# Performance work log

Hardware: AMD Instinct MI355X
Metric: run time of the kernel (lower is better)

Reference implementation:

```python
import jax, jax.numpy as jnp
import numpy as np

_EPS = 1e-5
RC = 5.0   # cutoff radius
L = 20     # number of radial basis functions
N = 10000  # nodes
E = 100000 # edges
F = 128    # in_feats


def _ssp(x):
    # ShiftedSoftplus: softplus(x) - log(2)
    return jax.nn.softplus(x) - jnp.log(2.0)


def _rbf(r):
    # DimeNet radial basis: sqrt(2/rc) * sin(n*pi*r/rc) / r, n = 1..L.  r: [E,1] -> [E,L]
    n = jnp.arange(1, L + 1, dtype=r.dtype)
    return jnp.sqrt(2.0 / RC) * jnp.sin(n * jnp.pi * r / RC) / r


def _fc(u):
    # cosine cutoff applied elementwise: 0.5*(cos(pi*u/rc)+1) for u < rc else 0
    return jnp.where(u < RC, 0.5 * (jnp.cos(jnp.pi * u / RC) + 1.0), 0.0)


def setup_inputs() -> dict:
    key = jax.random.key(0)
    ks = jax.random.split(key, 12)

    def nrm(k, shape, scale=1.0):
        return jax.random.normal(k, shape, dtype=jnp.float32) * scale

    return {
        "x": nrm(ks[0], (N, 3)) * 3.0,           # atomic positions
        "v": nrm(ks[1], (N, F, 3)),               # vector node features
        "s": nrm(ks[2], (N, F)),                  # scalar node features
        "ms1_w": nrm(ks[3], (F, F), F ** -0.5),
        "ms1_b": jnp.zeros((F,), jnp.float32),
        "ms2_w": nrm(ks[4], (3 * F, F), F ** -0.5),
        "ms2_b": jnp.zeros((3 * F,), jnp.float32),
        "mv_w": nrm(ks[5], (3 * F, L), L ** -0.5),
        "mv_b": jnp.zeros((3 * F,), jnp.float32),
        "us1_w": nrm(ks[6], (F, F), F ** -0.5),
        "us1_b": jnp.zeros((F,), jnp.float32),
        "us2_w": nrm(ks[7], (3 * F, F), F ** -0.5),
        "us2_b": jnp.zeros((3 * F,), jnp.float32),
        "src": jax.random.randint(ks[8], (E,), 0, N, dtype=jnp.int32),
        "dst": jax.random.randint(ks[9], (E,), 0, N, dtype=jnp.int32),
    }


def reference(x, v, s, ms1_w, ms1_b, ms2_w, ms2_b, mv_w, mv_b,
              us1_w, us1_b, us2_w, us2_b, src, dst):
    # ---------- pass 1: message1 + reduce1 (sum over incoming edges) ----------
    sj = s[src]                                   # [E,F]   src scalar features
    vj = v[src]                                   # [E,F,3] src vector features
    vec = x[src] - x[dst]                         # [E,3]   x_i - x_j (molecule branch)
    r = jnp.sqrt(jnp.sum(vec ** 2, axis=-1) + _EPS)[:, None]          # [E,1]
    phi = _ssp(sj @ ms1_w.T + ms1_b) @ ms2_w.T + ms2_b                 # [E,3F]
    w = _fc(_rbf(r) @ mv_w.T + mv_b)                                    # [E,3F]
    v_, s_, r_ = jnp.split(phi * w, 3, axis=-1)                         # each [E,F]
    dv_e = vj * v_[:, :, None] + r_[:, :, None] * (vec / r)[:, None, :] # [E,F,3]
    dv = jax.ops.segment_sum(dv_e, dst, num_segments=N)                 # [N,F,3]
    ds = jax.ops.segment_sum(s_, dst, num_segments=N)                   # [N,F]
    v_new = v + dv
    s_new = s + ds

    # ---------- pass 2: message2 + reduce2 (mean over incoming edges) ----------
    s2 = _ssp(s_new[src] @ us1_w.T + us1_b) @ us2_w.T + us2_b           # [E,3F]
    deg = jax.ops.segment_sum(jnp.ones((E,), s.dtype), dst, num_segments=N)
    denom = jnp.maximum(deg, 1.0)
    s_mean = jax.ops.segment_sum(s2, dst, num_segments=N) / denom[:, None]        # [N,3F]
    uv = jax.ops.segment_sum(v_new[src], dst, num_segments=N) / denom[:, None, None]  # [N,F,3]
    avv, asv, ass = jnp.split(s_mean, 3, axis=-1)                       # each [N,F]
    norm = jnp.sqrt(jnp.sum(uv ** 2, axis=-1) + _EPS)[..., None]        # [N,F,1]
    dv2 = uv * avv[:, :, None]                                           # [N,F,3]
    ds2 = jnp.sum((uv / norm) ** 2, axis=-1) * asv + ass                 # [N,F]
    return (v_new + dv2, s_new + ds2)
```

## Files before the change

### kernel.cpp

```cpp
#include <hip/hip_runtime.h>
#include <hip/hip_bf16.h>


#define F_DIM   128
#define F3_DIM  384
#define L_DIM   20
#define CAP     64

typedef __attribute__((ext_vector_type(8))) short short8;
typedef __attribute__((ext_vector_type(4))) float f32x4;
typedef __attribute__((ext_vector_type(4))) unsigned short us4;

__device__ __forceinline__ unsigned short f2bf(float f) {
  union { float f; unsigned u; } a; a.f = f;
  unsigned u = a.u;
  u = (u + 0x7FFFu + ((u >> 16) & 1u)) >> 16;
  return (unsigned short)u;
}
__device__ __forceinline__ float bf2f(unsigned short u) {
  union { unsigned u; float f; } a; a.u = ((unsigned)u) << 16;
  return a.f;
}

__global__ __launch_bounds__(256) void cast_kernel(
    const float* __restrict__ ms1_w, unsigned short* __restrict__ w_ms1,
    const float* __restrict__ ms2_w, unsigned short* __restrict__ w_ms2,
    const float* __restrict__ us1_w, unsigned short* __restrict__ w_us1,
    const float* __restrict__ us2_w, unsigned short* __restrict__ w_us2,
    const float* __restrict__ s,     unsigned short* __restrict__ sbf,
    const float* __restrict__ v,     us4* __restrict__ v4,
    const float* __restrict__ mv_w,  unsigned short* __restrict__ mvwB,
    int nF)
{
  int i = blockIdx.x * 256 + threadIdx.x;
  if (i < 16384) w_ms1[i] = f2bf(ms1_w[i]);
  if (i < 49152) w_ms2[i] = f2bf(ms2_w[i]);
  if (i < 16384) w_us1[i] = f2bf(us1_w[i]);
  if (i < 49152) w_us2[i] = f2bf(us2_w[i]);
  if (i < nF)    sbf[i] = f2bf(s[i]);
  if (i < nF) {
    const float* vp = v + (size_t)i * 3;
    us4 o; o.x = f2bf(vp[0]); o.y = f2bf(vp[1]); o.z = f2bf(vp[2]); o.w = 0;
    v4[i] = o;
  }
  if (i < 384 * 32) {
    int o = i >> 5, k = i & 31;
    float val = (k < 20) ? mv_w[o * 20 + k] * 0.6324555320336759f : 0.f;
    mvwB[i] = f2bf(val);
  }
}

__global__ __launch_bounds__(256) void fill_kernel(
    const int* __restrict__ src, const int* __restrict__ dst,
    int* __restrict__ cursor, int* __restrict__ jbuf, int E)
{
  int e = blockIdx.x * 256 + threadIdx.x;
  if (e < E) {
    int d = dst[e];
    int p = atomicAdd(&cursor[d], 1);
    if (p < CAP) jbuf[d * CAP + p] = src[e];
  }
}

__global__ __launch_bounds__(64) void mlp_kernel(
    const unsigned short* __restrict__ X,
    const unsigned short* __restrict__ W1,
    const float* __restrict__ B1,
    const unsigned short* __restrict__ W2,
    const float* __restrict__ B2,
    unsigned short* __restrict__ Yp)
{
  __shared__ float HT[128 * 17];
  const int lane = threadIdx.x;
  const int c    = lane & 15;
  const int quad = lane >> 4;
  const int m0   = blockIdx.x * 16;

  f32x4 acc[8];
#pragma unroll
  for (int t = 0; t < 8; t++) acc[t] = (f32x4){0.f, 0.f, 0.f, 0.f};
#pragma unroll
  for (int kk = 0; kk < 4; kk++) {
    short8 a = *(const short8*)(X + (size_t)(m0 + c) * 128 + kk * 32 + quad * 8);
#pragma unroll
    for (int t = 0; t < 8; t++) {
      short8 b = *(const short8*)(W1 + (size_t)(t * 16 + c) * 128 + kk * 32 + quad * 8);
      acc[t] = __builtin_amdgcn_mfma_f32_16x16x32_bf16(a, b, acc[t], 0, 0, 0);
    }
  }
#pragma unroll
  for (int t = 0; t < 8; t++) {
    float bias = B1[t * 16 + c];
    int k = t * 16 + c;
#pragma unroll
    for (int r = 0; r < 4; r++) {
      float h = acc[t][r] + bias;
      float sp = (h > 15.f) ? h : log1pf(__expf(h));
      sp -= 0.69314718056f;
      HT[k * 17 + quad * 4 + r] = sp;
    }
  }
  __syncthreads();

  for (int g = 0; g < 3; g++) {
    f32x4 acc2[8];
#pragma unroll
    for (int t = 0; t < 8; t++) acc2[t] = (f32x4){0.f, 0.f, 0.f, 0.f};
#pragma unroll
    for (int kk = 0; kk < 4; kk++) {
      short8 afr;
#pragma unroll
      for (int j = 0; j < 8; j++) {
        float hv = HT[(kk * 32 + quad * 8 + j) * 17 + c];
        afr[j] = (short)f2bf(hv);
      }
#pragma unroll
      for (int t = 0; t < 8; t++) {
        short8 b = *(const short8*)(W2 + (size_t)(g * 128 + t * 16 + c) * 128 + kk * 32 + quad * 8);
        acc2[t] = __builtin_amdgcn_mfma_f32_16x16x32_bf16(afr, b, acc2[t], 0, 0, 0);
      }
    }
#pragma unroll
    for (int t = 0; t < 8; t++) {
      int f = t * 16 + c;
      float bias = B2[g * 128 + f];
#pragma unroll
      for (int r = 0; r < 4; r++) {
        int m = quad * 4 + r;
        Yp[(size_t)(m0 + m) * 512 + f * 4 + g] = f2bf(acc2[t][r] + bias);
      }
    }
  }
}

__global__ __launch_bounds__(256, 4) void pass1_kernel(
    const float* __restrict__ x,
    const us4*  __restrict__ phi4,
    const us4*  __restrict__ v4,
    const float* __restrict__ v,
    const float* __restrict__ s,
    const unsigned short* __restrict__ mvwB,
    const float* __restrict__ mv_b,
    const int* __restrict__ jbuf,
    const int* __restrict__ deg,
    float* __restrict__ vnew, us4* __restrict__ vnew4,
    float* __restrict__ snew, unsigned short* __restrict__ snew_bf, int nNodes)
{
  __shared__ unsigned short Asn[32 * 32];
  __shared__ float4 Au[32];
  __shared__ us4 Wl[32 * 128];
  __shared__ float red[512];

  const int tid  = threadIdx.x;
  const int wave = tid >> 6, lane = tid & 63;
  const int half = wave >> 1, split = wave & 1;
  const int i = blockIdx.x;
  const int f = lane + 64 * half;
  const int c = lane & 15, quad = lane >> 4;

  int cnt = deg[i]; if (cnt > CAP) cnt = CAP;
  const int base = i * CAP;

  short8 bfr[6]; float bias[6];
#pragma unroll
  for (int p = 0; p < 3; p++)
#pragma unroll
    for (int h = 0; h < 2; h++) {
      int t = 2 * wave + h + 8 * p;
      bfr[p * 2 + h]  = *(const short8*)(mvwB + (size_t)(t * 16 + c) * 32 + quad * 8);
      bias[p * 2 + h] = mv_b[t * 16 + c];
    }

  const float xi0 = x[i * 3], xi1 = x[i * 3 + 1], xi2 = x[i * 3 + 2];
  int jv = (lane < cnt) ? jbuf[base + lane] : 0;

  float accV0 = 0.f, accV1 = 0.f, accV2 = 0.f, accS = 0.f;

  for (int bs = 0; bs < cnt; bs += 32) {
    int bcnt = cnt - bs; if (bcnt > 32) bcnt = 32;
    __syncthreads();

    if (tid < 32) {
      int e = bs + tid;
      if (e < cnt) {
        int j = jbuf[base + e];
        float d0 = x[j * 3]     - xi0;
        float d1 = x[j * 3 + 1] - xi1;
        float d2 = x[j * 3 + 2] - xi2;
        float r = sqrtf(d0 * d0 + d1 * d1 + d2 * d2 + 1e-5f);
        float invr = 1.0f / r;
        Au[tid] = make_float4(d0 * invr, d1 * invr, d2 * invr, invr);
        float theta = r * 0.6283185307179586f;
        float s1, c1;
        __sincosf(theta, &s1, &c1);
        float c2 = 2.f * c1;
        float pm2 = s1, pm1 = c2 * s1;
        Asn[tid * 32 + 0] = f2bf(pm2);
        Asn[tid * 32 + 1] = f2bf(pm1);
#pragma unroll
        for (int l = 2; l < L_DIM; l++) {
          float cur = c2 * pm1 - pm2;
          Asn[tid * 32 + l] = f2bf(cur);
          pm2 = pm1; pm1 = cur;
        }
#pragma unroll
        for (int l = L_DIM; l < 32; l++) Asn[tid * 32 + l] = 0;
      }
    }
    __syncthreads();

    int nrg = (bcnt + 15) >> 4;
    for (int rg = 0; rg < nrg; rg++) {
      short8 a = *(const short8*)&Asn[(rg * 16 + c) * 32 + quad * 8];
      f32x4 acc[6];
#pragma unroll
      for (int q = 0; q < 6; q++)
        acc[q] = __builtin_amdgcn_mfma_f32_16x16x32_bf16(
            a, bfr[q], (f32x4){0.f, 0.f, 0.f, 0.f}, 0, 0, 0);
#pragma unroll
      for (int r = 0; r < 4; r++) {
        int el = rg * 16 + quad * 4 + r;
        if (el < bcnt) {
          float invr = Au[el].w;
#pragma unroll
          for (int h = 0; h < 2; h++) {
            float wp0 = fmaf(acc[h][r],     invr, bias[h]);
            float wp1 = fmaf(acc[2 + h][r], invr, bias[2 + h]);
            float wp2 = fmaf(acc[4 + h][r], invr, bias[4 + h]);
            float w0 = (wp0 < 5.f) ? 0.5f * (__cosf(wp0 * 0.6283185307179586f) + 1.f) : 0.f;
            float w1 = (wp1 < 5.f) ? 0.5f * (__cosf(wp1 * 0.6283185307179586f) + 1.f) : 0.f;
            float w2 = (wp2 < 5.f) ? 0.5f * (__cosf(wp2 * 0.6283185307179586f) + 1.f) : 0.f;
            us4 o; o.x = f2bf(w0); o.y = f2bf(w1); o.z = f2bf(w2); o.w = 0;
            Wl[el * 128 + wave * 32 + h * 16 + c] = o;
          }
        }
      }
    }
    __syncthreads();

    for (int e = split; e < bcnt; e += 2) {
      int j = __shfl(jv, bs + e);
      float4 u = Au[e];
      us4 wv = Wl[e * 128 + f];
      us4 pv = phi4[(size_t)j * 128 + f];
      us4 vv = v4[(size_t)j * 128 + f];
      float m0 = bf2f(pv.x) * bf2f(wv.x);
      float m1 = bf2f(pv.y) * bf2f(wv.y);
      float m2 = bf2f(pv.z) * bf2f(wv.z);
      accV0 = fmaf(bf2f(vv.x), m0, fmaf(m2, u.x, accV0));
      accV1 = fmaf(bf2f(vv.y), m0, fmaf(m2, u.y, accV1));
      accV2 = fmaf(bf2f(vv.z), m0, fmaf(m2, u.z, accV2));
      accS += m1;
    }
  }

  const int idx = half * 64 + lane;
  __syncthreads();
  if (split == 1) {
    red[idx * 4 + 0] = accV0; red[idx * 4 + 1] = accV1;
    red[idx * 4 + 2] = accV2; red[idx * 4 + 3] = accS;
  }
  __syncthreads();
  if (split == 0) {
    accV0 += red[idx * 4 + 0]; accV1 += red[idx * 4 + 1];
    accV2 += red[idx * 4 + 2]; accS  += red[idx * 4 + 3];
    size_t b3 = (size_t)i * 384 + f * 3;
    float n0 = v[b3] + accV0, n1 = v[b3 + 1] + accV1, n2 = v[b3 + 2] + accV2;
    vnew[b3] = n0; vnew[b3 + 1] = n1; vnew[b3 + 2] = n2;
    us4 o; o.x = f2bf(n0); o.y = f2bf(n1); o.z = f2bf(n2); o.w = 0;
    vnew4[(size_t)i * 128 + f] = o;
    size_t b1 = (size_t)i * 128 + f;
    float sv = s[b1] + accS;
    snew[b1] = sv;
    snew_bf[b1] = f2bf(sv);
  }
}

__global__ __launch_bounds__(256, 8) void pass2_kernel(
    const float* __restrict__ vnew,
    const us4*  __restrict__ vnew4,
    const float* __restrict__ snew,
    const us4*  __restrict__ s2p,
    const int* __restrict__ jbuf, const int* __restrict__ deg,
    float* __restrict__ vout, float* __restrict__ sout, int nNodes)
{
  __shared__ float red[1024];
  const int wave = threadIdx.x >> 6, lane = threadIdx.x & 63;
  const int half = wave >> 1, split = wave & 1;
  const int i = blockIdx.x;
  const int f = lane + 64 * half;

  int cnt = deg[i]; if (cnt > CAP) cnt = CAP;
  const int base = i * CAP;
  int jv = (lane < cnt) ? jbuf[base + lane] : 0;

  float accU0 = 0.f, accU1 = 0.f, accU2 = 0.f;
  float accM0 = 0.f, accM1 = 0.f, accM2 = 0.f;

#pragma unroll 2
  for (int e = split; e < cnt; e += 2) {
    int j = __shfl(jv, e);
    us4 sm = s2p[(size_t)j * 128 + f];
    us4 vm = vnew4[(size_t)j * 128 + f];
    accM0 += bf2f(sm.x); accM1 += bf2f(sm.y); accM2 += bf2f(sm.z);
    accU0 += bf2f(vm.x); accU1 += bf2f(vm.y); accU2 += bf2f(vm.z);
  }

  const int idx = half * 64 + lane;
  if (split == 1) {
    red[idx * 8 + 0] = accU0; red[idx * 8 + 1] = accU1; red[idx * 8 + 2] = accU2;
    red[idx * 8 + 3] = accM0; red[idx * 8 + 4] = accM1; red[idx * 8 + 5] = accM2;
  }
  __syncthreads();
  if (split == 0) {
    accU0 += red[idx * 8 + 0]; accU1 += red[idx * 8 + 1]; accU2 += red[idx * 8 + 2];
    accM0 += red[idx * 8 + 3]; accM1 += red[idx * 8 + 4]; accM2 += red[idx * 8 + 5];

    float dinv = 1.0f / (float)(cnt > 0 ? cnt : 1);
    float uv0 = accU0 * dinv, uv1 = accU1 * dinv, uv2 = accU2 * dinv;
    float avv = accM0 * dinv, asv = accM1 * dinv, ass = accM2 * dinv;
    float q = uv0 * uv0 + uv1 * uv1 + uv2 * uv2;
    float ds2 = (q / (q + 1e-5f)) * asv + ass;
    size_t b3 = (size_t)i * 384 + f * 3;
    vout[b3]     = vnew[b3]     + uv0 * avv;
    vout[b3 + 1] = vnew[b3 + 1] + uv1 * avv;
    vout[b3 + 2] = vnew[b3 + 2] + uv2 * avv;
    size_t b1 = (size_t)i * 128 + f;
    sout[b1] = snew[b1] + ds2;
  }
}

extern "C" void kernel_launch(void* const* d_in, const int* in_sizes, int n_in,
                              void* d_out, int out_size, void* d_ws, size_t ws_size,
                              hipStream_t stream)
{
  const float* x     = (const float*)d_in[0];
  const float* v     = (const float*)d_in[1];
  const float* s     = (const float*)d_in[2];
  const float* ms1_w = (const float*)d_in[3];
  const float* ms1_b = (const float*)d_in[4];
  const float* ms2_w = (const float*)d_in[5];
  const float* ms2_b = (const float*)d_in[6];
  const float* mv_w  = (const float*)d_in[7];
  const float* mv_b  = (const float*)d_in[8];
  const float* us1_w = (const float*)d_in[9];
  const float* us1_b = (const float*)d_in[10];
  const float* us2_w = (const float*)d_in[11];
  const float* us2_b = (const float*)d_in[12];
  const int*   src   = (const int*)d_in[13];
  const int*   dst   = (const int*)d_in[14];

  const int N = in_sizes[0] / 3;
  const int E = in_sizes[13];

  char* p = (char*)d_ws;
  auto alloc = [&](size_t bytes) -> void* {
    void* r = (void*)p;
    p += (bytes + 255) & ~(size_t)255;
    return r;
  };
  unsigned short* sbf   = (unsigned short*)alloc((size_t)N * 128 * 2);
  unsigned short* snbf  = (unsigned short*)alloc((size_t)N * 128 * 2);
  unsigned short* w_ms1 = (unsigned short*)alloc(16384 * 2);
  unsigned short* w_ms2 = (unsigned short*)alloc(49152 * 2);
  unsigned short* w_us1 = (unsigned short*)alloc(16384 * 2);
  unsigned short* w_us2 = (unsigned short*)alloc(49152 * 2);
  unsigned short* mvwB  = (unsigned short*)alloc(384 * 32 * 2);
  us4*   phi4   = (us4*)alloc((size_t)N * 128 * 8);
  us4*   v4     = (us4*)alloc((size_t)N * 128 * 8);
  us4*   vnew4  = (us4*)alloc((size_t)N * 128 * 8);
  us4*   s2p    = (us4*)alloc((size_t)N * 128 * 8);
  float* vnew   = (float*)alloc((size_t)N * 384 * 4);
  float* snew   = (float*)alloc((size_t)N * 128 * 4);
  int* cursor   = (int*)alloc((size_t)N * 4);
  int* jbuf     = (int*)alloc((size_t)N * CAP * 4);

  hipMemsetAsync(cursor, 0, (size_t)N * 4, stream);

  cast_kernel<<<(N * 128 + 255) / 256, 256, 0, stream>>>(
      ms1_w, w_ms1, ms2_w, w_ms2, us1_w, w_us1, us2_w, w_us2,
      s, sbf, v, v4, mv_w, mvwB, N * 128);

  fill_kernel<<<(E + 255) / 256, 256, 0, stream>>>(src, dst, cursor, jbuf, E);

  mlp_kernel<<<N / 16, 64, 0, stream>>>(sbf, w_ms1, ms1_b, w_ms2, ms2_b,
                                        (unsigned short*)phi4);

  pass1_kernel<<<N, 256, 0, stream>>>(x, phi4, v4, v, s, mvwB, mv_b,
                                      jbuf, cursor, vnew, vnew4, snew, snbf, N);

  mlp_kernel<<<N / 16, 64, 0, stream>>>(snbf, w_us1, us1_b, w_us2, us2_b,
                                        (unsigned short*)s2p);

  float* vout = (float*)d_out;
  float* sout = vout + (size_t)N * 384;
  pass2_kernel<<<N, 256, 0, stream>>>(vnew, vnew4, snew, s2p, jbuf, cursor,
                                      vout, sout, N);
}
```

Before: 260.1 us.

## Pack per-node phi and vector features into combined 12-byte gather records

The MLP kernels now write their three bf16 outputs interleaved with the node's bf16 vector features into one 12-byte record per (node, feature). The edge-gather loops in pass1 and pass2 then do a single 12-byte load instead of two 8-byte loads from separate arrays, which drops the padding slot and halves the number of gather streams. Other changes: the cast and fill kernels are merged into one launch, the second MLP stage computes all three output groups in a single loop, and pass1 takes source indices from a lane shuffle instead of reloading them from jbuf. The cost is an extra read of v4/vnew4 in the MLP kernels and 12-byte loads that may not be aligned to 16 bytes.

```diff
diff --git a/kernel.cpp b/kernel.cpp
--- a/kernel.cpp
+++ b/kernel.cpp
@@ -10,6 +10,8 @@
 typedef __attribute__((ext_vector_type(8))) short short8;
 typedef __attribute__((ext_vector_type(4))) float f32x4;
 typedef __attribute__((ext_vector_type(4))) unsigned short us4;
+
+struct u3 { unsigned a, b, c; };
 
 __device__ __forceinline__ unsigned short f2bf(float f) {
   union { float f; unsigned u; } a; a.f = f;
@@ -22,7 +24,7 @@
   return a.f;
 }
 
-__global__ __launch_bounds__(256) void cast_kernel(
+__global__ __launch_bounds__(256) void cast_fill_kernel(
     const float* __restrict__ ms1_w, unsigned short* __restrict__ w_ms1,
     const float* __restrict__ ms2_w, unsigned short* __restrict__ w_ms2,
     const float* __restrict__ us1_w, unsigned short* __restrict__ w_us1,
@@ -30,7 +32,9 @@
     const float* __restrict__ s,     unsigned short* __restrict__ sbf,
     const float* __restrict__ v,     us4* __restrict__ v4,
     const float* __restrict__ mv_w,  unsigned short* __restrict__ mvwB,
-    int nF)
+    const int* __restrict__ src, const int* __restrict__ dst,
+    int* __restrict__ cursor, int* __restrict__ jbuf,
+    int nF, int E)
 {
   int i = blockIdx.x * 256 + threadIdx.x;
   if (i < 16384) w_ms1[i] = f2bf(ms1_w[i]);
@@ -48,17 +52,10 @@
     float val = (k < 20) ? mv_w[o * 20 + k] * 0.6324555320336759f : 0.f;
     mvwB[i] = f2bf(val);
   }
-}
-
-__global__ __launch_bounds__(256) void fill_kernel(
-    const int* __restrict__ src, const int* __restrict__ dst,
-    int* __restrict__ cursor, int* __restrict__ jbuf, int E)
-{
-  int e = blockIdx.x * 256 + threadIdx.x;
-  if (e < E) {
-    int d = dst[e];
+  if (i < E) {
+    int d = dst[i];
     int p = atomicAdd(&cursor[d], 1);
-    if (p < CAP) jbuf[d * CAP + p] = src[e];
+    if (p < CAP) jbuf[d * CAP + p] = src[i];
   }
 }
 
@@ -68,7 +65,8 @@
     const float* __restrict__ B1,
     const unsigned short* __restrict__ W2,
     const float* __restrict__ B2,
-    unsigned short* __restrict__ Yp)
+    const us4* __restrict__ Vin,
+    unsigned short* __restrict__ Yc)
 {
   __shared__ float HT[128 * 17];
   const int lane = threadIdx.x;
@@ -102,41 +100,50 @@
   }
   __syncthreads();
 
-  for (int g = 0; g < 3; g++) {
-    f32x4 acc2[8];
-#pragma unroll
-    for (int t = 0; t < 8; t++) acc2[t] = (f32x4){0.f, 0.f, 0.f, 0.f};
-#pragma unroll
-    for (int kk = 0; kk < 4; kk++) {
-      short8 afr;
-#pragma unroll
-      for (int j = 0; j < 8; j++) {
-        float hv = HT[(kk * 32 + quad * 8 + j) * 17 + c];
-        afr[j] = (short)f2bf(hv);
-      }
+  f32x4 acc2[3][8];
+#pragma unroll
+  for (int g = 0; g < 3; g++)
+#pragma unroll
+    for (int t = 0; t < 8; t++) acc2[g][t] = (f32x4){0.f, 0.f, 0.f, 0.f};
+#pragma unroll
+  for (int kk = 0; kk < 4; kk++) {
+    short8 afr;
+#pragma unroll
+    for (int j = 0; j < 8; j++) {
+      float hv = HT[(kk * 32 + quad * 8 + j) * 17 + c];
+      afr[j] = (short)f2bf(hv);
+    }
+#pragma unroll
+    for (int g = 0; g < 3; g++)
 #pragma unroll
       for (int t = 0; t < 8; t++) {
         short8 b = *(const short8*)(W2 + (size_t)(g * 128 + t * 16 + c) * 128 + kk * 32 + quad * 8);
-        acc2[t] = __builtin_amdgcn_mfma_f32_16x16x32_bf16(afr, b, acc2[t], 0, 0, 0);
+        acc2[g][t] = __builtin_amdgcn_mfma_f32_16x16x32_bf16(afr, b, acc2[g][t], 0, 0, 0);
       }
-    }
-#pragma unroll
-    for (int t = 0; t < 8; t++) {
-      int f = t * 16 + c;
-      float bias = B2[g * 128 + f];
-#pragma unroll
-      for (int r = 0; r < 4; r++) {
-        int m = quad * 4 + r;
-        Yp[(size_t)(m0 + m) * 512 + f * 4 + g] = f2bf(acc2[t][r] + bias);
-      }
+  }
+#pragma unroll
+  for (int t = 0; t < 8; t++) {
+    int f = t * 16 + c;
+    float b0 = B2[f], b1 = B2[128 + f], b2 = B2[256 + f];
+#pragma unroll
+    for (int r = 0; r < 4; r++) {
+      int m = quad * 4 + r;
+      us4 vv = Vin[(size_t)(m0 + m) * 128 + f];
+      unsigned p0 = f2bf(acc2[0][t][r] + b0);
+      unsigned p1 = f2bf(acc2[1][t][r] + b1);
+      unsigned p2 = f2bf(acc2[2][t][r] + b2);
+      u3 rec;
+      rec.a = p0 | (p1 << 16);
+      rec.b = p2 | ((unsigned)vv.x << 16);
+      rec.c = (unsigned)vv.y | ((unsigned)vv.z << 16);
+      *(u3*)(Yc + ((size_t)(m0 + m) * 128 + f) * 6) = rec;
     }
   }
 }
 
 __global__ __launch_bounds__(256, 4) void pass1_kernel(
     const float* __restrict__ x,
-    const us4*  __restrict__ phi4,
-    const us4*  __restrict__ v4,
+    const unsigned short* __restrict__ combo1,
     const float* __restrict__ v,
     const float* __restrict__ s,
     const unsigned short* __restrict__ mvwB,
@@ -182,8 +189,8 @@
 
     if (tid < 32) {
       int e = bs + tid;
+      int j = __shfl(jv, e);
       if (e < cnt) {
-        int j = jbuf[base + e];
         float d0 = x[j * 3]     - xi0;
         float d1 = x[j * 3 + 1] - xi1;
         float d2 = x[j * 3 + 2] - xi2;
@@ -242,14 +249,19 @@
       int j = __shfl(jv, bs + e);
       float4 u = Au[e];
       us4 wv = Wl[e * 128 + f];
-      us4 pv = phi4[(size_t)j * 128 + f];
-      us4 vv = v4[(size_t)j * 128 + f];
-      float m0 = bf2f(pv.x) * bf2f(wv.x);
-      float m1 = bf2f(pv.y) * bf2f(wv.y);
-      float m2 = bf2f(pv.z) * bf2f(wv.z);
-      accV0 = fmaf(bf2f(vv.x), m0, fmaf(m2, u.x, accV0));
-      accV1 = fmaf(bf2f(vv.y), m0, fmaf(m2, u.y, accV1));
-      accV2 = fmaf(bf2f(vv.z), m0, fmaf(m2, u.z, accV2));
+      u3 cb = *(const u3*)(combo1 + ((size_t)j * 128 + f) * 6);
+      float ph0 = bf2f((unsigned short)(cb.a & 0xffff));
+      float ph1 = bf2f((unsigned short)(cb.a >> 16));
+      float ph2 = bf2f((unsigned short)(cb.b & 0xffff));
+      float vx  = bf2f((unsigned short)(cb.b >> 16));
+      float vy  = bf2f((unsigned short)(cb.c & 0xffff));
+      float vz  = bf2f((unsigned short)(cb.c >> 16));
+      float m0 = ph0 * bf2f(wv.x);
+      float m1 = ph1 * bf2f(wv.y);
+      float m2 = ph2 * bf2f(wv.z);
+      accV0 = fmaf(vx, m0, fmaf(m2, u.x, accV0));
+      accV1 = fmaf(vy, m0, fmaf(m2, u.y, accV1));
+      accV2 = fmaf(vz, m0, fmaf(m2, u.z, accV2));
       accS += m1;
     }
   }
@@ -278,9 +290,8 @@
 
 __global__ __launch_bounds__(256, 8) void pass2_kernel(
     const float* __restrict__ vnew,
-    const us4*  __restrict__ vnew4,
     const float* __restrict__ snew,
-    const us4*  __restrict__ s2p,
+    const unsigned short* __restrict__ combo2,
     const int* __restrict__ jbuf, const int* __restrict__ deg,
     float* __restrict__ vout, float* __restrict__ sout, int nNodes)
 {
@@ -300,10 +311,13 @@
 #pragma unroll 2
   for (int e = split; e < cnt; e += 2) {
     int j = __shfl(jv, e);
-    us4 sm = s2p[(size_t)j * 128 + f];
-    us4 vm = vnew4[(size_t)j * 128 + f];
-    accM0 += bf2f(sm.x); accM1 += bf2f(sm.y); accM2 += bf2f(sm.z);
-    accU0 += bf2f(vm.x); accU1 += bf2f(vm.y); accU2 += bf2f(vm.z);
+    u3 cb = *(const u3*)(combo2 + ((size_t)j * 128 + f) * 6);
+    accM0 += bf2f((unsigned short)(cb.a & 0xffff));
+    accM1 += bf2f((unsigned short)(cb.a >> 16));
+    accM2 += bf2f((unsigned short)(cb.b & 0xffff));
+    accU0 += bf2f((unsigned short)(cb.b >> 16));
+    accU1 += bf2f((unsigned short)(cb.c & 0xffff));
+    accU2 += bf2f((unsigned short)(cb.c >> 16));
   }
 
   const int idx = half * 64 + lane;
@@ -366,10 +380,10 @@
   unsigned short* w_us1 = (unsigned short*)alloc(16384 * 2);
   unsigned short* w_us2 = (unsigned short*)alloc(49152 * 2);
   unsigned short* mvwB  = (unsigned short*)alloc(384 * 32 * 2);
-  us4*   phi4   = (us4*)alloc((size_t)N * 128 * 8);
   us4*   v4     = (us4*)alloc((size_t)N * 128 * 8);
   us4*   vnew4  = (us4*)alloc((size_t)N * 128 * 8);
-  us4*   s2p    = (us4*)alloc((size_t)N * 128 * 8);
+  unsigned short* combo1 = (unsigned short*)alloc((size_t)N * 128 * 12);
+  unsigned short* combo2 = (unsigned short*)alloc((size_t)N * 128 * 12);
   float* vnew   = (float*)alloc((size_t)N * 384 * 4);
   float* snew   = (float*)alloc((size_t)N * 128 * 4);
   int* cursor   = (int*)alloc((size_t)N * 4);
@@ -377,23 +391,21 @@
 
   hipMemsetAsync(cursor, 0, (size_t)N * 4, stream);
 
-  cast_kernel<<<(N * 128 + 255) / 256, 256, 0, stream>>>(
+  cast_fill_kernel<<<(N * 128 + 255) / 256, 256, 0, stream>>>(
       ms1_w, w_ms1, ms2_w, w_ms2, us1_w, w_us1, us2_w, w_us2,
-      s, sbf, v, v4, mv_w, mvwB, N * 128);
-
-  fill_kernel<<<(E + 255) / 256, 256, 0, stream>>>(src, dst, cursor, jbuf, E);
+      s, sbf, v, v4, mv_w, mvwB, src, dst, cursor, jbuf, N * 128, E);
 
   mlp_kernel<<<N / 16, 64, 0, stream>>>(sbf, w_ms1, ms1_b, w_ms2, ms2_b,
-                                        (unsigned short*)phi4);
-
-  pass1_kernel<<<N, 256, 0, stream>>>(x, phi4, v4, v, s, mvwB, mv_b,
+                                        v4, combo1);
+
+  pass1_kernel<<<N, 256, 0, stream>>>(x, combo1, v, s, mvwB, mv_b,
                                       jbuf, cursor, vnew, vnew4, snew, snbf, N);
 
   mlp_kernel<<<N / 16, 64, 0, stream>>>(snbf, w_us1, us1_b, w_us2, us2_b,
-                                        (unsigned short*)s2p);
+                                        vnew4, combo2);
 
   float* vout = (float*)d_out;
   float* sout = vout + (size_t)N * 384;
-  pass2_kernel<<<N, 256, 0, stream>>>(vnew, vnew4, snew, s2p, jbuf, cursor,
+  pass2_kernel<<<N, 256, 0, stream>>>(vnew, snew, combo2, jbuf, cursor,
                                       vout, sout, N);
 }
```

After: 248.2 us. -4.6%, faster.
